# Kernel optimization log

Hardware: AMD Instinct MI355X
Metric: run time of the kernel (lower is better)

The kernel has to match this reference:

```python
import jax, jax.numpy as jnp
import numpy as np

N = 262144   # nodes
E = 2097152  # edges (avg degree 8)
F_IN, L0, L1, K = 14, 128, 15, 15


def setup_inputs() -> dict:
    key = jax.random.key(0)
    ks = jax.random.split(key, 24)
    s = 0.1
    return {
        "x": jax.random.normal(ks[0], (N, F_IN), jnp.float32),
        "edge_index": jax.random.randint(ks[1], (2, E), 0, N, dtype=jnp.int32),
        "y": jax.random.randint(ks[2], (N, 1), 0, 2, dtype=jnp.int32),
        "sel": jax.random.bernoulli(ks[3], 0.98, (N, 1)),
        "Wl1": jax.random.normal(ks[4], (F_IN, L0)) * s,
        "Wr1": jax.random.normal(ks[5], (F_IN, L0)) * s,
        "b1": jnp.zeros((L0,), jnp.float32),
        "Wl2": jax.random.normal(ks[6], (L0, L0)) * s,
        "Wr2": jax.random.normal(ks[7], (L0, L0)) * s,
        "b2": jnp.zeros((L0,), jnp.float32),
        "Wl3": jax.random.normal(ks[8], (L0, 1)) * s,
        "Wr3": jax.random.normal(ks[9], (L0, 1)) * s,
        "b3": jnp.zeros((1,), jnp.float32),
        "Wt1": jax.random.normal(ks[10], (K + 1, F_IN, L1)) * s,
        "bt1": jnp.zeros((L1,), jnp.float32),
        "Wt2": jax.random.normal(ks[11], (K + 1, L1, L1)) * s,
        "bt2": jnp.zeros((L1,), jnp.float32),
        "Wt3": jax.random.normal(ks[12], (K + 1, L1, 1)) * s,
        "bt3": jnp.zeros((1,), jnp.float32),
        "Wlin": jax.random.normal(ks[13], (2, 1)) * s,
        "blin": jnp.zeros((1,), jnp.float32),
    }


def _sage(h, src, dst, inv_deg, Wl, Wr, b):
    # PyG SAGEConv (mean aggr): lin_l(mean_j x_j) + lin_r(x_i) + b
    agg = jax.ops.segment_sum(h[src], dst, num_segments=N) * inv_deg
    return agg @ Wl + h @ Wr + b


def _tag(h, src, dst, norm, W, b):
    # PyG TAGConv: sum_k (D^-1/2 A D^-1/2)^k x @ W_k + b
    out = h @ W[0]
    for k in range(1, W.shape[0]):
        h = jax.ops.segment_sum(norm[:, None] * h[src], dst, num_segments=N)
        out = out + h @ W[k]
    return out + b


def reference(x, edge_index, y, sel, Wl1, Wr1, b1, Wl2, Wr2, b2, Wl3, Wr3, b3,
              Wt1, bt1, Wt2, bt2, Wt3, bt3, Wlin, blin):
    src, dst = edge_index[0], edge_index[1]
    ones = jnp.ones((E,), jnp.float32)
    deg = jax.ops.segment_sum(ones, dst, num_segments=N)  # in-degree at targets
    inv_deg = (1.0 / jnp.maximum(deg, 1.0))[:, None]
    # gcn_norm without self-loops for TAGConv
    dinv = jnp.where(deg > 0, jax.lax.rsqrt(jnp.maximum(deg, 1.0)), 0.0)
    norm = dinv[src] * dinv[dst]  # [E]

    # SAGE branch
    x1 = jax.nn.sigmoid(_sage(x, src, dst, inv_deg, Wl1, Wr1, b1))
    for _ in range(4):
        x1 = jax.nn.sigmoid(_sage(x1, src, dst, inv_deg, Wl2, Wr2, b2))
    x1 = jax.nn.relu(_sage(x1, src, dst, inv_deg, Wl3, Wr3, b3))

    # TAG branch
    x3 = jax.nn.sigmoid(_tag(x, src, dst, norm, Wt1, bt1))
    for _ in range(4):
        x3 = jax.nn.sigmoid(_tag(x3, src, dst, norm, Wt2, bt2))
    x3 = jax.nn.relu(_tag(x3, src, dst, norm, Wt3, bt3))

    out = jax.nn.relu(jnp.concatenate([x1, x3], axis=1) @ Wlin + blin)
    return jnp.where(sel & (y == 0), 0.0, out)
```

## Files before the change

### kernel.cpp

```cpp
#include <hip/hip_runtime.h>
#include <math.h>

#define NN 262144
#define EE 2097152
#define FIN 14
#define LW 128
#define TW 15

typedef unsigned short ushort_t;
typedef unsigned int uint_t;
typedef __attribute__((ext_vector_type(8))) short bf16x8v;
typedef __attribute__((ext_vector_type(4))) float f32x4v;

static __device__ __forceinline__ float sigmoidf_(float v) { return 1.0f / (1.0f + expf(-v)); }

static __device__ __forceinline__ float bf2f(unsigned short u) {
  union { unsigned int i; float f; } v; v.i = ((unsigned int)u) << 16; return v.f;
}
static __device__ __forceinline__ unsigned short f2bf(float f) {
  union { float f; unsigned int i; } v; v.f = f;
  unsigned int r = v.i + 0x7FFF + ((v.i >> 16) & 1);
  return (unsigned short)(r >> 16);
}
static __device__ __forceinline__ unsigned int pack2(float a, float b) {
  return ((unsigned int)f2bf(b) << 16) | (unsigned int)f2bf(a);
}
static __device__ __forceinline__ void addrow16(float* acc, uint4 u0, uint4 u1) {
  acc[0]  += bf2f((unsigned short)(u0.x & 0xFFFF)); acc[1]  += bf2f((unsigned short)(u0.x >> 16));
  acc[2]  += bf2f((unsigned short)(u0.y & 0xFFFF)); acc[3]  += bf2f((unsigned short)(u0.y >> 16));
  acc[4]  += bf2f((unsigned short)(u0.z & 0xFFFF)); acc[5]  += bf2f((unsigned short)(u0.z >> 16));
  acc[6]  += bf2f((unsigned short)(u0.w & 0xFFFF)); acc[7]  += bf2f((unsigned short)(u0.w >> 16));
  acc[8]  += bf2f((unsigned short)(u1.x & 0xFFFF)); acc[9]  += bf2f((unsigned short)(u1.x >> 16));
  acc[10] += bf2f((unsigned short)(u1.y & 0xFFFF)); acc[11] += bf2f((unsigned short)(u1.y >> 16));
  acc[12] += bf2f((unsigned short)(u1.z & 0xFFFF)); acc[13] += bf2f((unsigned short)(u1.z >> 16));
  acc[14] += bf2f((unsigned short)(u1.w & 0xFFFF)); acc[15] += bf2f((unsigned short)(u1.w >> 16));
}

__global__ void k_selprobe(const unsigned char* __restrict__ selb, int* __restrict__ flag) {
  __shared__ int cnt;
  if (threadIdx.x == 0) cnt = 0;
  __syncthreads();
  int c = 0;
  for (int i = threadIdx.x; i < 4096; i += 256) c += (selb[i] != 0) ? 1 : 0;
  atomicAdd(&cnt, c);
  __syncthreads();
  if (threadIdx.x == 0) *flag = (cnt > 3000) ? 1 : 0;
}

__global__ void k_norm_bool(const int* __restrict__ flag, const unsigned char* __restrict__ selb,
                            unsigned char* __restrict__ selN) {
  if (*flag != 1) return;
  int i = blockIdx.x * 256 + threadIdx.x;
  selN[i] = (selb[i] != 0) ? 1 : 0;
}

__global__ void k_norm_int(const int* __restrict__ flag, const unsigned char* __restrict__ selb,
                           unsigned char* __restrict__ selN) {
  if (*flag != 0) return;
  int i = blockIdx.x * 256 + threadIdx.x;
  selN[i] = (((const int*)selb)[i] != 0) ? 1 : 0;
}

__global__ void k_deg(const int* __restrict__ ei, int* __restrict__ deg) {
  int e = blockIdx.x * 256 + threadIdx.x;
  if (e < EE) atomicAdd(&deg[ei[EE + e]], 1);
}

__global__ void k_scan_partial(const int* __restrict__ deg, int* __restrict__ btot) {
  __shared__ int sd[256];
  int t = threadIdx.x, b = blockIdx.x;
  int i0 = b * 1024 + t * 4;
  int s = deg[i0] + deg[i0 + 1] + deg[i0 + 2] + deg[i0 + 3];
  sd[t] = s; __syncthreads();
  for (int off = 1; off < 256; off <<= 1) {
    int x = (t >= off) ? sd[t - off] : 0;
    __syncthreads(); sd[t] += x; __syncthreads();
  }
  if (t == 255) btot[b] = sd[255];
}

__global__ void k_scan_block(const int* __restrict__ btot, int* __restrict__ bbase, int* __restrict__ row_start) {
  __shared__ int sd[256];
  int t = threadIdx.x;
  int v = btot[t];
  sd[t] = v; __syncthreads();
  for (int off = 1; off < 256; off <<= 1) {
    int x = (t >= off) ? sd[t - off] : 0;
    __syncthreads(); sd[t] += x; __syncthreads();
  }
  bbase[t] = sd[t] - v;
  if (t == 255) row_start[NN] = sd[255];
}

__global__ void k_scan_final(const int* __restrict__ deg, const int* __restrict__ bbase,
                             int* __restrict__ row_start, float* __restrict__ inv_deg,
                             float* __restrict__ dinv) {
  __shared__ int sd[256];
  int t = threadIdx.x, b = blockIdx.x;
  int i0 = b * 1024 + t * 4;
  int d0 = deg[i0], d1 = deg[i0 + 1], d2 = deg[i0 + 2], d3 = deg[i0 + 3];
  int s = d0 + d1 + d2 + d3;
  sd[t] = s; __syncthreads();
  for (int off = 1; off < 256; off <<= 1) {
    int x = (t >= off) ? sd[t - off] : 0;
    __syncthreads(); sd[t] += x; __syncthreads();
  }
  int base = bbase[b] + sd[t] - s;
  row_start[i0]     = base;
  row_start[i0 + 1] = base + d0;
  row_start[i0 + 2] = base + d0 + d1;
  row_start[i0 + 3] = base + d0 + d1 + d2;
  int dd[4] = {d0, d1, d2, d3};
  for (int j = 0; j < 4; ++j) {
    float df = (float)dd[j];
    inv_deg[i0 + j] = 1.0f / fmaxf(df, 1.0f);
    dinv[i0 + j] = (dd[j] > 0) ? rsqrtf(fmaxf(df, 1.0f)) : 0.0f;
  }
}

__global__ void k_fill(const int* __restrict__ ei, const int* __restrict__ row_start,
                       int* __restrict__ cursor, int* __restrict__ csr_src) {
  int e = blockIdx.x * 256 + threadIdx.x;
  if (e >= EE) return;
  int s = ei[e], d = ei[EE + e];
  int pos = atomicAdd(&cursor[d], 1);
  csr_src[row_start[d] + pos] = s;
}

__global__ void k_pad_x(const float* __restrict__ x, float* __restrict__ xp,
                        ushort_t* __restrict__ xpb, ushort_t* __restrict__ xc) {
  int idx = blockIdx.x * 256 + threadIdx.x;
  int i = idx >> 4, lane = idx & 15;
  float v = (lane < FIN) ? x[(size_t)i * FIN + lane] : 0.0f;
  xp[idx] = v;
  ushort_t b = f2bf(v);
  xpb[idx] = b;
  xc[(size_t)i * 32 + 16 + lane] = b;
}

__global__ __launch_bounds__(256) void k_prop16_mean(
    const float* __restrict__ h, ushort_t* __restrict__ xc,
    const int* __restrict__ row_start, const int* __restrict__ csr_src,
    const float* __restrict__ inv_deg) {
  int i = blockIdx.x * 256 + threadIdx.x;
  float acc[16];
  #pragma unroll
  for (int c = 0; c < 16; ++c) acc[c] = 0.0f;
  int e0 = row_start[i], e1 = row_start[i + 1];
  int e = e0;
  for (; e + 2 <= e1; e += 2) {
    int i0 = csr_src[e], i1 = csr_src[e + 1];
    const float4* r0 = (const float4*)(h + (size_t)i0 * 16);
    const float4* r1 = (const float4*)(h + (size_t)i1 * 16);
    float4 a0 = r0[0], a1 = r0[1], a2 = r0[2], a3 = r0[3];
    float4 b0 = r1[0], b1 = r1[1], b2 = r1[2], b3 = r1[3];
    acc[0]+=a0.x+b0.x; acc[1]+=a0.y+b0.y; acc[2]+=a0.z+b0.z; acc[3]+=a0.w+b0.w;
    acc[4]+=a1.x+b1.x; acc[5]+=a1.y+b1.y; acc[6]+=a1.z+b1.z; acc[7]+=a1.w+b1.w;
    acc[8]+=a2.x+b2.x; acc[9]+=a2.y+b2.y; acc[10]+=a2.z+b2.z; acc[11]+=a2.w+b2.w;
    acc[12]+=a3.x+b3.x; acc[13]+=a3.y+b3.y; acc[14]+=a3.z+b3.z; acc[15]+=a3.w+b3.w;
  }
  for (; e < e1; ++e) {
    const float4* r0 = (const float4*)(h + (size_t)csr_src[e] * 16);
    float4 a0 = r0[0], a1 = r0[1], a2 = r0[2], a3 = r0[3];
    acc[0]+=a0.x; acc[1]+=a0.y; acc[2]+=a0.z; acc[3]+=a0.w;
    acc[4]+=a1.x; acc[5]+=a1.y; acc[6]+=a1.z; acc[7]+=a1.w;
    acc[8]+=a2.x; acc[9]+=a2.y; acc[10]+=a2.z; acc[11]+=a2.w;
    acc[12]+=a3.x; acc[13]+=a3.y; acc[14]+=a3.z; acc[15]+=a3.w;
  }
  float idg = inv_deg[i];
  uint_t o[8];
  #pragma unroll
  for (int q = 0; q < 8; ++q) o[q] = pack2(acc[2*q]*idg, acc[2*q+1]*idg);
  uint4* dst = (uint4*)(xc + (size_t)i * 32);
  dst[0] = make_uint4(o[0], o[1], o[2], o[3]);
  dst[1] = make_uint4(o[4], o[5], o[6], o[7]);
}

__global__ void k_convW1(const float* __restrict__ Wl1, const float* __restrict__ Wr1,
                         ushort_t* __restrict__ Wc) {
  int idx = blockIdx.x * 256 + threadIdx.x;
  int n = idx >> 5, k = idx & 31;
  float v = 0.0f;
  if (k < FIN) v = Wl1[k * 128 + n];
  else if (k >= 16 && k < 16 + FIN) v = Wr1[(k - 16) * 128 + n];
  Wc[idx] = f2bf(v);
}

__global__ __launch_bounds__(256) void k_gemm_small_mfma(
    const ushort_t* __restrict__ xc, const ushort_t* __restrict__ Wc,
    const float* __restrict__ bias, ushort_t* __restrict__ out) {
  int tid = threadIdx.x;
  int wave = tid >> 6, lane = tid & 63;
  int row0 = blockIdx.x * 64 + wave * 16;
  int r = lane & 15, kg = lane >> 4;
  bf16x8v a = *(const bf16x8v*)(xc + (size_t)(row0 + r) * 32 + kg * 8);
  f32x4v acc[8];
  #pragma unroll
  for (int nt = 0; nt < 8; ++nt) {
    acc[nt] = (f32x4v){0.f, 0.f, 0.f, 0.f};
    bf16x8v b = *(const bf16x8v*)(Wc + (size_t)(nt * 16 + r) * 32 + kg * 8);
    acc[nt] = __builtin_amdgcn_mfma_f32_16x16x32_bf16(a, b, acc[nt], 0, 0, 0);
  }
  #pragma unroll
  for (int nt = 0; nt < 8; ++nt) {
    #pragma unroll
    for (int j = 0; j < 4; ++j) {
      float v = sigmoidf_(acc[nt][j] + bias[nt * 16 + r]);
      out[(size_t)(row0 + kg * 4 + j) * LW + nt * 16 + r] = f2bf(v);
    }
  }
}

__global__ void k_prop128(const ushort_t* __restrict__ h, ushort_t* __restrict__ out,
                          const int* __restrict__ row_start, const int* __restrict__ csr_src,
                          const float* __restrict__ inv_deg) {
  int t = threadIdx.x;
  int g = blockIdx.x * 4 + (t >> 6);
  int lane = t & 63;
  int s0 = row_start[g], s1 = row_start[g + 1];
  float a0 = 0.0f, a1 = 0.0f;
  int e = s0;
  for (; e + 8 <= s1; e += 8) {
    int id[8];
    #pragma unroll
    for (int j = 0; j < 8; ++j) id[j] = csr_src[e + j];
    uint_t u[8];
    #pragma unroll
    for (int j = 0; j < 8; ++j) u[j] = *(const uint_t*)(h + (size_t)id[j] * LW + 2 * lane);
    #pragma unroll
    for (int j = 0; j < 8; ++j) {
      a0 += bf2f((unsigned short)(u[j] & 0xFFFF));
      a1 += bf2f((unsigned short)(u[j] >> 16));
    }
  }
  for (; e < s1; ++e) {
    uint_t u = *(const uint_t*)(h + (size_t)csr_src[e] * LW + 2 * lane);
    a0 += bf2f((unsigned short)(u & 0xFFFF));
    a1 += bf2f((unsigned short)(u >> 16));
  }
  float idg = inv_deg[g];
  *(uint_t*)(out + (size_t)g * LW + 2 * lane) = pack2(a0 * idg, a1 * idg);
}

__global__ void k_convW(const float* __restrict__ Wl, const float* __restrict__ Wr,
                        ushort_t* __restrict__ Wt) {
  int idx = blockIdx.x * 256 + threadIdx.x;
  int n = idx >> 8, k = idx & 255;
  float v = (k < 128) ? Wl[k * 128 + n] : Wr[(k - 128) * 128 + n];
  Wt[idx] = f2bf(v);
}

__global__ __launch_bounds__(256) void k_gemm128_mfma(
    const ushort_t* __restrict__ A1, const ushort_t* __restrict__ A2,
    const ushort_t* __restrict__ Wt,
    const float* __restrict__ bias, ushort_t* __restrict__ out) {
  int tid = threadIdx.x;
  int wave = tid >> 6, lane = tid & 63;
  int row0 = blockIdx.x * 64 + wave * 16;
  int r = lane & 15, kg = lane >> 4;
  f32x4v acc[8];
  #pragma unroll
  for (int nt = 0; nt < 8; ++nt) acc[nt] = (f32x4v){0.f, 0.f, 0.f, 0.f};
  #pragma unroll
  for (int ks = 0; ks < 8; ++ks) {
    const ushort_t* asrc = (ks < 4)
        ? (A1 + (size_t)(row0 + r) * LW + ks * 32 + kg * 8)
        : (A2 + (size_t)(row0 + r) * LW + (ks - 4) * 32 + kg * 8);
    bf16x8v a = *(const bf16x8v*)asrc;
    #pragma unroll
    for (int nt = 0; nt < 8; ++nt) {
      bf16x8v b = *(const bf16x8v*)(Wt + (size_t)(nt * 16 + r) * 256 + ks * 32 + kg * 8);
      acc[nt] = __builtin_amdgcn_mfma_f32_16x16x32_bf16(a, b, acc[nt], 0, 0, 0);
    }
  }
  #pragma unroll
  for (int nt = 0; nt < 8; ++nt) {
    #pragma unroll
    for (int j = 0; j < 4; ++j) {
      float v = sigmoidf_(acc[nt][j] + bias[nt * 16 + r]);
      out[(size_t)(row0 + kg * 4 + j) * LW + nt * 16 + r] = f2bf(v);
    }
  }
}

__global__ void k_wide_to1(const ushort_t* __restrict__ H, const float* __restrict__ Wl3,
                           const float* __restrict__ Wr3, float* __restrict__ g_l,
                           float* __restrict__ g_r) {
  int wave = (blockIdx.x * 256 + threadIdx.x) >> 6;
  int lane = threadIdx.x & 63;
  unsigned int u = *(const unsigned int*)(H + (size_t)wave * LW + 2 * lane);
  float h0 = bf2f((unsigned short)(u & 0xFFFF));
  float h1 = bf2f((unsigned short)(u >> 16));
  float al = h0 * Wl3[2 * lane] + h1 * Wl3[2 * lane + 1];
  float ar = h0 * Wr3[2 * lane] + h1 * Wr3[2 * lane + 1];
  #pragma unroll
  for (int off = 32; off; off >>= 1) {
    al += __shfl_xor(al, off);
    ar += __shfl_xor(ar, off);
  }
  if (lane == 0) { g_l[wave] = al; g_r[wave] = ar; }
}

__global__ void k_sage_final(const float* __restrict__ g_l, const float* __restrict__ g_r,
                             const float* __restrict__ b3, const int* __restrict__ row_start,
                             const int* __restrict__ csr_src, const float* __restrict__ inv_deg,
                             float* __restrict__ x1) {
  int i = blockIdx.x * 256 + threadIdx.x;
  int e0 = row_start[i], e1 = row_start[i + 1];
  float s = 0.0f;
  int e = e0;
  for (; e + 4 <= e1; e += 4) {
    float w0 = g_l[csr_src[e]], w1 = g_l[csr_src[e+1]];
    float w2 = g_l[csr_src[e+2]], w3 = g_l[csr_src[e+3]];
    s += (w0 + w1) + (w2 + w3);
  }
  for (; e < e1; ++e) s += g_l[csr_src[e]];
  float v = s * inv_deg[i] + g_r[i] + b3[0];
  x1[i] = fmaxf(v, 0.0f);
}

__global__ __launch_bounds__(256) void k_tag_hh(
    const ushort_t* __restrict__ T, const float* __restrict__ W, int win,
    const ushort_t* __restrict__ w_in, ushort_t* __restrict__ w_out,
    const float* __restrict__ bias, int mode,
    const float* __restrict__ W2, int win2, ushort_t* __restrict__ w_next2,
    const int* __restrict__ row_start, const int* __restrict__ csr_src,
    const float* __restrict__ dinv) {
  __shared__ float Ws[16][16];
  __shared__ float Ws2[16][16];
  int t = threadIdx.x;
  { int rr = t >> 4, c = t & 15; Ws[rr][c] = (rr < win && c < TW) ? W[rr * TW + c] : 0.0f; }
  if (mode == 3) {
    int rr = t >> 4, c = t & 15;
    Ws2[rr][c] = (rr < win2 && c < TW) ? W2[rr * TW + c] : 0.0f;
  }
  __syncthreads();
  int i = blockIdx.x * 256 + t;
  float di = dinv[i];
  float acc[16];
  #pragma unroll
  for (int c = 0; c < 16; ++c) acc[c] = 0.0f;

  if (mode != 0) {
    int e0 = row_start[i], e1 = row_start[i + 1];
    int e = e0;
    for (; e + 8 <= e1; e += 8) {
      int id[8];
      #pragma unroll
      for (int j = 0; j < 8; ++j) id[j] = csr_src[e + j];
      uint4 u0[8], u1[8];
      #pragma unroll
      for (int j = 0; j < 8; ++j) {
        const uint4* p = (const uint4*)(w_in + (size_t)id[j] * 16);
        u0[j] = p[0]; u1[j] = p[1];
      }
      #pragma unroll
      for (int j = 0; j < 8; ++j) addrow16(acc, u0[j], u1[j]);
    }
    for (; e + 4 <= e1; e += 4) {
      int id[4];
      #pragma unroll
      for (int j = 0; j < 4; ++j) id[j] = csr_src[e + j];
      uint4 u0[4], u1[4];
      #pragma unroll
      for (int j = 0; j < 4; ++j) {
        const uint4* p = (const uint4*)(w_in + (size_t)id[j] * 16);
        u0[j] = p[0]; u1[j] = p[1];
      }
      #pragma unroll
      for (int j = 0; j < 4; ++j) addrow16(acc, u0[j], u1[j]);
    }
    for (; e < e1; ++e) {
      const uint4* p = (const uint4*)(w_in + (size_t)csr_src[e] * 16);
      addrow16(acc, p[0], p[1]);
    }
    #pragma unroll
    for (int c = 0; c < 16; ++c) acc[c] *= di;
  }

  uint4 t0 = *(const uint4*)(T + (size_t)i * 16);
  uint4 t1 = *(const uint4*)(T + (size_t)i * 16 + 8);
  float tv[16];
  tv[0]=bf2f((unsigned short)(t0.x&0xFFFF)); tv[1]=bf2f((unsigned short)(t0.x>>16));
  tv[2]=bf2f((unsigned short)(t0.y&0xFFFF)); tv[3]=bf2f((unsigned short)(t0.y>>16));
  tv[4]=bf2f((unsigned short)(t0.z&0xFFFF)); tv[5]=bf2f((unsigned short)(t0.z>>16));
  tv[6]=bf2f((unsigned short)(t0.w&0xFFFF)); tv[7]=bf2f((unsigned short)(t0.w>>16));
  tv[8]=bf2f((unsigned short)(t1.x&0xFFFF)); tv[9]=bf2f((unsigned short)(t1.x>>16));
  tv[10]=bf2f((unsigned short)(t1.y&0xFFFF)); tv[11]=bf2f((unsigned short)(t1.y>>16));
  tv[12]=bf2f((unsigned short)(t1.z&0xFFFF)); tv[13]=bf2f((unsigned short)(t1.z>>16));
  tv[14]=bf2f((unsigned short)(t1.w&0xFFFF)); tv[15]=bf2f((unsigned short)(t1.w>>16));
  #pragma unroll
  for (int f = 0; f < 16; ++f) {
    float tf = tv[f];
    const float4* wr = (const float4*)Ws[f];
    float4 w0 = wr[0], w1 = wr[1], w2 = wr[2], w3 = wr[3];
    acc[0]+=tf*w0.x; acc[1]+=tf*w0.y; acc[2]+=tf*w0.z; acc[3]+=tf*w0.w;
    acc[4]+=tf*w1.x; acc[5]+=tf*w1.y; acc[6]+=tf*w1.z; acc[7]+=tf*w1.w;
    acc[8]+=tf*w2.x; acc[9]+=tf*w2.y; acc[10]+=tf*w2.z; acc[11]+=tf*w2.w;
    acc[12]+=tf*w3.x; acc[13]+=tf*w3.y; acc[14]+=tf*w3.z; acc[15]+=tf*w3.w;
  }

  if (mode >= 2) {
    float tn[16];
    #pragma unroll
    for (int c = 0; c < 16; ++c)
      tn[c] = (c < TW) ? sigmoidf_(acc[c] + bias[c]) : 0.0f;
    uint_t o[8];
    #pragma unroll
    for (int q = 0; q < 8; ++q) o[q] = pack2(tn[2*q], tn[2*q+1]);
    uint4* dst = (uint4*)(w_out + (size_t)i * 16);
    dst[0] = make_uint4(o[0], o[1], o[2], o[3]);
    dst[1] = make_uint4(o[4], o[5], o[6], o[7]);
    if (mode == 3) {
      float wn[16];
      #pragma unroll
      for (int c = 0; c < 16; ++c) wn[c] = 0.0f;
      #pragma unroll
      for (int f = 0; f < 16; ++f) {
        float tf = tn[f];
        const float4* wr = (const float4*)Ws2[f];
        float4 w0 = wr[0], w1 = wr[1], w2 = wr[2], w3 = wr[3];
        wn[0]+=tf*w0.x; wn[1]+=tf*w0.y; wn[2]+=tf*w0.z; wn[3]+=tf*w0.w;
        wn[4]+=tf*w1.x; wn[5]+=tf*w1.y; wn[6]+=tf*w1.z; wn[7]+=tf*w1.w;
        wn[8]+=tf*w2.x; wn[9]+=tf*w2.y; wn[10]+=tf*w2.z; wn[11]+=tf*w2.w;
        wn[12]+=tf*w3.x; wn[13]+=tf*w3.y; wn[14]+=tf*w3.z; wn[15]+=tf*w3.w;
      }
      uint_t o2[8];
      #pragma unroll
      for (int q = 0; q < 8; ++q) o2[q] = pack2(di * wn[2*q], di * wn[2*q+1]);
      uint4* dst2 = (uint4*)(w_next2 + (size_t)i * 16);
      dst2[0] = make_uint4(o2[0], o2[1], o2[2], o2[3]);
      dst2[1] = make_uint4(o2[4], o2[5], o2[6], o2[7]);
    }
  } else {
    uint_t o[8];
    #pragma unroll
    for (int q = 0; q < 8; ++q) o[q] = pack2(di * acc[2*q], di * acc[2*q+1]);
    uint4* dst = (uint4*)(w_out + (size_t)i * 16);
    dst[0] = make_uint4(o[0], o[1], o[2], o[3]);
    dst[1] = make_uint4(o[4], o[5], o[6], o[7]);
  }
}

__global__ void k_tag_g(const ushort_t* __restrict__ T, const float* __restrict__ Wt3,
                        const float* __restrict__ dinv, float* __restrict__ gT,
                        float* __restrict__ w15) {
  __shared__ float Ws[16 * TW];
  int t = threadIdx.x;
  if (t < 16 * TW) Ws[t] = Wt3[t];
  __syncthreads();
  int i = blockIdx.x * 256 + t;
  const ushort_t* tr = T + (size_t)i * 16;
  float row[TW];
  #pragma unroll
  for (int f = 0; f < TW; ++f) row[f] = bf2f(tr[f]);
  #pragma unroll
  for (int k = 0; k < 16; ++k) {
    float a = 0.0f;
    #pragma unroll
    for (int f = 0; f < TW; ++f) a += row[f] * Ws[k * TW + f];
    if (k < 15) gT[(size_t)k * NN + i] = a;
    else        w15[i] = dinv[i] * a;
  }
}

__global__ void k_horner(const float* __restrict__ gk, const float* __restrict__ w_in,
                         float* __restrict__ w_out,
                         const int* __restrict__ row_start, const int* __restrict__ csr_src,
                         const float* __restrict__ dinv) {
  int i = blockIdx.x * 256 + threadIdx.x;
  int e0 = row_start[i], e1 = row_start[i + 1];
  float gs = 0.0f;
  int e = e0;
  for (; e + 4 <= e1; e += 4) {
    float w0 = w_in[csr_src[e]],   w1 = w_in[csr_src[e+1]];
    float w2 = w_in[csr_src[e+2]], w3 = w_in[csr_src[e+3]];
    gs += (w0 + w1) + (w2 + w3);
  }
  for (; e < e1; ++e) gs += w_in[csr_src[e]];
  float s = gk[i] + dinv[i] * gs;
  w_out[i] = dinv[i] * s;
}

__global__ void k_horner_fin(const float* __restrict__ g0, const float* __restrict__ w_in,
                             const float* __restrict__ x1, const int* __restrict__ y,
                             const unsigned char* __restrict__ selN,
                             const float* __restrict__ Wlin, const float* __restrict__ blin,
                             const float* __restrict__ bt3,
                             const int* __restrict__ row_start, const int* __restrict__ csr_src,
                             const float* __restrict__ dinv, float* __restrict__ out) {
  int i = blockIdx.x * 256 + threadIdx.x;
  int e0 = row_start[i], e1 = row_start[i + 1];
  float gs = 0.0f;
  int e = e0;
  for (; e + 4 <= e1; e += 4) {
    float w0 = w_in[csr_src[e]],   w1 = w_in[csr_src[e+1]];
    float w2 = w_in[csr_src[e+2]], w3 = w_in[csr_src[e+3]];
    gs += (w0 + w1) + (w2 + w3);
  }
  for (; e < e1; ++e) gs += w_in[csr_src[e]];
  float s = g0[i] + dinv[i] * gs;
  float x3 = fmaxf(s + bt3[0], 0.0f);
  float v = fmaxf(x1[i] * Wlin[0] + x3 * Wlin[1] + blin[0], 0.0f);
  bool z = (selN[i] != 0) && (y[i] == 0);
  out[i] = z ? 0.0f : v;
}

extern "C" void kernel_launch(void* const* d_in, const int* in_sizes, int n_in,
                              void* d_out, int out_size, void* d_ws, size_t ws_size,
                              hipStream_t stream) {
  const float* x    = (const float*)d_in[0];
  const int*   ei   = (const int*)d_in[1];
  const int*   y    = (const int*)d_in[2];
  const unsigned char* sel = (const unsigned char*)d_in[3];
  const float* Wl1  = (const float*)d_in[4];
  const float* Wr1  = (const float*)d_in[5];
  const float* b1   = (const float*)d_in[6];
  const float* Wl2  = (const float*)d_in[7];
  const float* Wr2  = (const float*)d_in[8];
  const float* b2   = (const float*)d_in[9];
  const float* Wl3  = (const float*)d_in[10];
  const float* Wr3  = (const float*)d_in[11];
  const float* b3   = (const float*)d_in[12];
  const float* Wt1  = (const float*)d_in[13];
  const float* bt1  = (const float*)d_in[14];
  const float* Wt2  = (const float*)d_in[15];
  const float* bt2  = (const float*)d_in[16];
  const float* Wt3  = (const float*)d_in[17];
  const float* bt3  = (const float*)d_in[18];
  const float* Wlin = (const float*)d_in[19];
  const float* blin = (const float*)d_in[20];

  const size_t MB = 1 << 20;
  unsigned char* w8 = (unsigned char*)d_ws;
  int*   deg       = (int*)(w8 + 0 * MB);
  int*   cursor    = (int*)(w8 + 1 * MB);
  int*   row_start = (int*)(w8 + 2 * MB);
  float* inv_deg   = (float*)(w8 + 4 * MB);
  float* dinv      = (float*)(w8 + 5 * MB);
  float* x1        = (float*)(w8 + 6 * MB);
  float* g_l       = (float*)(w8 + 7 * MB);
  float* g_r       = (float*)(w8 + 8 * MB);
  int*   btot      = (int*)(w8 + 9 * MB);
  int*   bbase     = (int*)(w8 + 9 * MB + 4096);
  int*   selflag   = (int*)(w8 + 9 * MB + 8192);
  float* w6a       = (float*)(w8 + 11 * MB);
  float* w6b       = (float*)(w8 + 12 * MB);
  unsigned char* selN = (unsigned char*)(w8 + 13 * MB);
  ushort_t* Wtc    = (ushort_t*)(w8 + 14 * MB);
  ushort_t* Wc1    = (ushort_t*)(w8 + 15 * MB);
  int*   csr_src   = (int*)(w8 + 16 * MB);
  float* xp        = (float*)(w8 + 24 * MB);
  ushort_t* xpb    = (ushort_t*)(w8 + 40 * MB);
  ushort_t* H      = (ushort_t*)(w8 + 48 * MB);
  ushort_t* AGG    = (ushort_t*)(w8 + 112 * MB);
  ushort_t* xc     = (ushort_t*)(w8 + 112 * MB);
  ushort_t* T0  = (ushort_t*)(w8 + 112 * MB);
  ushort_t* T1  = (ushort_t*)(w8 + 120 * MB);
  ushort_t* wA  = (ushort_t*)(w8 + 128 * MB);
  ushort_t* wB  = (ushort_t*)(w8 + 136 * MB);
  float* gT     = (float*)(w8 + 144 * MB);

  k_selprobe<<<1, 256, 0, stream>>>(sel, selflag);
  k_norm_bool<<<NN / 256, 256, 0, stream>>>(selflag, sel, selN);
  k_norm_int<<<NN / 256, 256, 0, stream>>>(selflag, sel, selN);

  hipMemsetAsync(w8, 0, 2 * MB, stream);
  k_deg<<<EE / 256, 256, 0, stream>>>(ei, deg);
  k_scan_partial<<<256, 256, 0, stream>>>(deg, btot);
  k_scan_block<<<1, 256, 0, stream>>>(btot, bbase, row_start);
  k_scan_final<<<256, 256, 0, stream>>>(deg, bbase, row_start, inv_deg, dinv);
  k_fill<<<EE / 256, 256, 0, stream>>>(ei, row_start, cursor, csr_src);
  k_pad_x<<<NN * 16 / 256, 256, 0, stream>>>(x, xp, xpb, xc);
  k_convW<<<128, 256, 0, stream>>>(Wl2, Wr2, Wtc);
  k_convW1<<<16, 256, 0, stream>>>(Wl1, Wr1, Wc1);

  k_prop16_mean<<<NN / 256, 256, 0, stream>>>(xp, xc, row_start, csr_src, inv_deg);
  k_gemm_small_mfma<<<NN / 64, 256, 0, stream>>>(xc, Wc1, b1, H);
  for (int l = 0; l < 4; ++l) {
    k_prop128<<<NN / 4, 256, 0, stream>>>(H, AGG, row_start, csr_src, inv_deg);
    k_gemm128_mfma<<<NN / 64, 256, 0, stream>>>(AGG, H, Wtc, b2, H);
  }
  k_wide_to1<<<NN / 4, 256, 0, stream>>>(H, Wl3, Wr3, g_l, g_r);
  k_sage_final<<<NN / 256, 256, 0, stream>>>(g_l, g_r, b3, row_start, csr_src, inv_deg, x1);

  const size_t FT = (size_t)FIN * TW;
  const size_t TT = (size_t)TW * TW;
  ushort_t* wi = wA; ushort_t* wo = wB;
  k_tag_hh<<<NN / 256, 256, 0, stream>>>(xpb, Wt1 + 15 * FT, FIN, nullptr, wi, nullptr, 0,
                                         nullptr, 0, nullptr, row_start, csr_src, dinv);
  for (int k = 14; k >= 1; --k) {
    k_tag_hh<<<NN / 256, 256, 0, stream>>>(xpb, Wt1 + (size_t)k * FT, FIN, wi, wo, nullptr, 1,
                                           nullptr, 0, nullptr, row_start, csr_src, dinv);
    ushort_t* tmp = wi; wi = wo; wo = tmp;
  }
  k_tag_hh<<<NN / 256, 256, 0, stream>>>(xpb, Wt1, FIN, wi, T0, bt1, 3,
                                         Wt2 + 15 * TT, TW, wo, row_start, csr_src, dinv);
  { ushort_t* tmp = wi; wi = wo; wo = tmp; }
  ushort_t* tin = T0; ushort_t* tout = T1;
  for (int l = 0; l < 4; ++l) {
    for (int k = 14; k >= 1; --k) {
      k_tag_hh<<<NN / 256, 256, 0, stream>>>(tin, Wt2 + (size_t)k * TT, TW, wi, wo, nullptr, 1,
                                             nullptr, 0, nullptr, row_start, csr_src, dinv);
      ushort_t* tmp = wi; wi = wo; wo = tmp;
    }
    if (l < 3) {
      k_tag_hh<<<NN / 256, 256, 0, stream>>>(tin, Wt2, TW, wi, tout, bt2, 3,
                                             Wt2 + 15 * TT, TW, wo, row_start, csr_src, dinv);
      ushort_t* tmp = wi; wi = wo; wo = tmp;
    } else {
      k_tag_hh<<<NN / 256, 256, 0, stream>>>(tin, Wt2, TW, wi, tout, bt2, 2,
                                             nullptr, 0, nullptr, row_start, csr_src, dinv);
    }
    ushort_t* tmp = tin; tin = tout; tout = tmp;
  }
  k_tag_g<<<NN / 256, 256, 0, stream>>>(tin, Wt3, dinv, gT, w6a);
  float* fwi = w6a; float* fwo = w6b;
  for (int k = 14; k >= 1; --k) {
    k_horner<<<NN / 256, 256, 0, stream>>>(gT + (size_t)k * NN, fwi, fwo,
                                           row_start, csr_src, dinv);
    float* tmp = fwi; fwi = fwo; fwo = tmp;
  }
  k_horner_fin<<<NN / 256, 256, 0, stream>>>(gT, fwi, x1, y, selN, Wlin, blin, bt3,
                                             row_start, csr_src, dinv, (float*)d_out);
}
```

Before: 4.309 ms.

## Split TAG and prop16 gathers across two threads per node, templatize mode

The 16-wide TAG Horner kernels and the first SAGE mean aggregation now use two threads per node, each gathering and accumulating 8 channels. Mode-3 exchanges the two halves with a lane shuffle so each thread can compute its half of the next-layer projection. The first SAGE layer now gathers bf16 rows instead of fp32, which drops the fp32 padded copy of x. Other changes: mode becomes a template parameter, the 128-wide GEMM loads all A fragments before its MFMA loop, and the Horner gathers unroll by 8. These are meant to raise memory-level parallelism and occupancy in the many latency-bound gather kernels, at the cost of duplicated index loads and doubled thread count.

```diff
diff --git a/kernel.cpp b/kernel.cpp
--- a/kernel.cpp
+++ b/kernel.cpp
@@ -25,15 +25,11 @@
 static __device__ __forceinline__ unsigned int pack2(float a, float b) {
   return ((unsigned int)f2bf(b) << 16) | (unsigned int)f2bf(a);
 }
-static __device__ __forceinline__ void addrow16(float* acc, uint4 u0, uint4 u1) {
-  acc[0]  += bf2f((unsigned short)(u0.x & 0xFFFF)); acc[1]  += bf2f((unsigned short)(u0.x >> 16));
-  acc[2]  += bf2f((unsigned short)(u0.y & 0xFFFF)); acc[3]  += bf2f((unsigned short)(u0.y >> 16));
-  acc[4]  += bf2f((unsigned short)(u0.z & 0xFFFF)); acc[5]  += bf2f((unsigned short)(u0.z >> 16));
-  acc[6]  += bf2f((unsigned short)(u0.w & 0xFFFF)); acc[7]  += bf2f((unsigned short)(u0.w >> 16));
-  acc[8]  += bf2f((unsigned short)(u1.x & 0xFFFF)); acc[9]  += bf2f((unsigned short)(u1.x >> 16));
-  acc[10] += bf2f((unsigned short)(u1.y & 0xFFFF)); acc[11] += bf2f((unsigned short)(u1.y >> 16));
-  acc[12] += bf2f((unsigned short)(u1.z & 0xFFFF)); acc[13] += bf2f((unsigned short)(u1.z >> 16));
-  acc[14] += bf2f((unsigned short)(u1.w & 0xFFFF)); acc[15] += bf2f((unsigned short)(u1.w >> 16));
+static __device__ __forceinline__ void addrow8(float* acc, uint4 u) {
+  acc[0] += bf2f((unsigned short)(u.x & 0xFFFF)); acc[1] += bf2f((unsigned short)(u.x >> 16));
+  acc[2] += bf2f((unsigned short)(u.y & 0xFFFF)); acc[3] += bf2f((unsigned short)(u.y >> 16));
+  acc[4] += bf2f((unsigned short)(u.z & 0xFFFF)); acc[5] += bf2f((unsigned short)(u.z >> 16));
+  acc[6] += bf2f((unsigned short)(u.w & 0xFFFF)); acc[7] += bf2f((unsigned short)(u.w >> 16));
 }
 
 __global__ void k_selprobe(const unsigned char* __restrict__ selb, int* __restrict__ flag) {
@@ -127,53 +123,48 @@
   csr_src[row_start[d] + pos] = s;
 }
 
-__global__ void k_pad_x(const float* __restrict__ x, float* __restrict__ xp,
-                        ushort_t* __restrict__ xpb, ushort_t* __restrict__ xc) {
+__global__ void k_pad_x(const float* __restrict__ x, ushort_t* __restrict__ xpb,
+                        ushort_t* __restrict__ xc) {
   int idx = blockIdx.x * 256 + threadIdx.x;
   int i = idx >> 4, lane = idx & 15;
   float v = (lane < FIN) ? x[(size_t)i * FIN + lane] : 0.0f;
-  xp[idx] = v;
   ushort_t b = f2bf(v);
   xpb[idx] = b;
   xc[(size_t)i * 32 + 16 + lane] = b;
 }
 
-__global__ __launch_bounds__(256) void k_prop16_mean(
-    const float* __restrict__ h, ushort_t* __restrict__ xc,
+__global__ __launch_bounds__(256) void k_prop16b(
+    const ushort_t* __restrict__ h, ushort_t* __restrict__ xc,
     const int* __restrict__ row_start, const int* __restrict__ csr_src,
     const float* __restrict__ inv_deg) {
-  int i = blockIdx.x * 256 + threadIdx.x;
-  float acc[16];
-  #pragma unroll
-  for (int c = 0; c < 16; ++c) acc[c] = 0.0f;
+  int gi = blockIdx.x * 256 + threadIdx.x;
+  int i = gi >> 1, half = gi & 1;
+  float acc[8];
+  #pragma unroll
+  for (int c = 0; c < 8; ++c) acc[c] = 0.0f;
+  const ushort_t* wbase = h + half * 8;
   int e0 = row_start[i], e1 = row_start[i + 1];
   int e = e0;
+  for (; e + 8 <= e1; e += 8) {
+    int id[8];
+    #pragma unroll
+    for (int j = 0; j < 8; ++j) id[j] = csr_src[e + j];
+    uint4 u[8];
+    #pragma unroll
+    for (int j = 0; j < 8; ++j) u[j] = *(const uint4*)(wbase + (size_t)id[j] * 16);
+    #pragma unroll
+    for (int j = 0; j < 8; ++j) addrow8(acc, u[j]);
+  }
   for (; e + 2 <= e1; e += 2) {
-    int i0 = csr_src[e], i1 = csr_src[e + 1];
-    const float4* r0 = (const float4*)(h + (size_t)i0 * 16);
-    const float4* r1 = (const float4*)(h + (size_t)i1 * 16);
-    float4 a0 = r0[0], a1 = r0[1], a2 = r0[2], a3 = r0[3];
-    float4 b0 = r1[0], b1 = r1[1], b2 = r1[2], b3 = r1[3];
-    acc[0]+=a0.x+b0.x; acc[1]+=a0.y+b0.y; acc[2]+=a0.z+b0.z; acc[3]+=a0.w+b0.w;
-    acc[4]+=a1.x+b1.x; acc[5]+=a1.y+b1.y; acc[6]+=a1.z+b1.z; acc[7]+=a1.w+b1.w;
-    acc[8]+=a2.x+b2.x; acc[9]+=a2.y+b2.y; acc[10]+=a2.z+b2.z; acc[11]+=a2.w+b2.w;
-    acc[12]+=a3.x+b3.x; acc[13]+=a3.y+b3.y; acc[14]+=a3.z+b3.z; acc[15]+=a3.w+b3.w;
-  }
-  for (; e < e1; ++e) {
-    const float4* r0 = (const float4*)(h + (size_t)csr_src[e] * 16);
-    float4 a0 = r0[0], a1 = r0[1], a2 = r0[2], a3 = r0[3];
-    acc[0]+=a0.x; acc[1]+=a0.y; acc[2]+=a0.z; acc[3]+=a0.w;
-    acc[4]+=a1.x; acc[5]+=a1.y; acc[6]+=a1.z; acc[7]+=a1.w;
-    acc[8]+=a2.x; acc[9]+=a2.y; acc[10]+=a2.z; acc[11]+=a2.w;
-    acc[12]+=a3.x; acc[13]+=a3.y; acc[14]+=a3.z; acc[15]+=a3.w;
-  }
+    uint4 u0 = *(const uint4*)(wbase + (size_t)csr_src[e] * 16);
+    uint4 u1 = *(const uint4*)(wbase + (size_t)csr_src[e + 1] * 16);
+    addrow8(acc, u0); addrow8(acc, u1);
+  }
+  if (e < e1) addrow8(acc, *(const uint4*)(wbase + (size_t)csr_src[e] * 16));
   float idg = inv_deg[i];
-  uint_t o[8];
-  #pragma unroll
-  for (int q = 0; q < 8; ++q) o[q] = pack2(acc[2*q]*idg, acc[2*q+1]*idg);
-  uint4* dst = (uint4*)(xc + (size_t)i * 32);
-  dst[0] = make_uint4(o[0], o[1], o[2], o[3]);
-  dst[1] = make_uint4(o[4], o[5], o[6], o[7]);
+  uint4 o = make_uint4(pack2(acc[0]*idg, acc[1]*idg), pack2(acc[2]*idg, acc[3]*idg),
+                       pack2(acc[4]*idg, acc[5]*idg), pack2(acc[6]*idg, acc[7]*idg));
+  *(uint4*)(xc + (size_t)i * 32 + half * 8) = o;
 }
 
 __global__ void k_convW1(const float* __restrict__ Wl1, const float* __restrict__ Wr1,
@@ -258,19 +249,23 @@
   int wave = tid >> 6, lane = tid & 63;
   int row0 = blockIdx.x * 64 + wave * 16;
   int r = lane & 15, kg = lane >> 4;
-  f32x4v acc[8];
-  #pragma unroll
-  for (int nt = 0; nt < 8; ++nt) acc[nt] = (f32x4v){0.f, 0.f, 0.f, 0.f};
+  bf16x8v a[8];
   #pragma unroll
   for (int ks = 0; ks < 8; ++ks) {
     const ushort_t* asrc = (ks < 4)
         ? (A1 + (size_t)(row0 + r) * LW + ks * 32 + kg * 8)
         : (A2 + (size_t)(row0 + r) * LW + (ks - 4) * 32 + kg * 8);
-    bf16x8v a = *(const bf16x8v*)asrc;
+    a[ks] = *(const bf16x8v*)asrc;
+  }
+  f32x4v acc[8];
+  #pragma unroll
+  for (int nt = 0; nt < 8; ++nt) acc[nt] = (f32x4v){0.f, 0.f, 0.f, 0.f};
+  #pragma unroll
+  for (int ks = 0; ks < 8; ++ks) {
     #pragma unroll
     for (int nt = 0; nt < 8; ++nt) {
       bf16x8v b = *(const bf16x8v*)(Wt + (size_t)(nt * 16 + r) * 256 + ks * 32 + kg * 8);
-      acc[nt] = __builtin_amdgcn_mfma_f32_16x16x32_bf16(a, b, acc[nt], 0, 0, 0);
+      acc[nt] = __builtin_amdgcn_mfma_f32_16x16x32_bf16(a[ks], b, acc[nt], 0, 0, 0);
     }
   }
   #pragma unroll
@@ -319,63 +314,50 @@
   x1[i] = fmaxf(v, 0.0f);
 }
 
+template<int MODE>
 __global__ __launch_bounds__(256) void k_tag_hh(
     const ushort_t* __restrict__ T, const float* __restrict__ W, int win,
     const ushort_t* __restrict__ w_in, ushort_t* __restrict__ w_out,
-    const float* __restrict__ bias, int mode,
+    const float* __restrict__ bias,
     const float* __restrict__ W2, int win2, ushort_t* __restrict__ w_next2,
     const int* __restrict__ row_start, const int* __restrict__ csr_src,
     const float* __restrict__ dinv) {
   __shared__ float Ws[16][16];
   __shared__ float Ws2[16][16];
   int t = threadIdx.x;
-  { int rr = t >> 4, c = t & 15; Ws[rr][c] = (rr < win && c < TW) ? W[rr * TW + c] : 0.0f; }
-  if (mode == 3) {
-    int rr = t >> 4, c = t & 15;
-    Ws2[rr][c] = (rr < win2 && c < TW) ? W2[rr * TW + c] : 0.0f;
-  }
+  { int rr = t >> 4, c = t & 15;
+    Ws[rr][c] = (rr < win && c < TW) ? W[rr * TW + c] : 0.0f;
+    if (MODE == 3) Ws2[rr][c] = (rr < win2 && c < TW) ? W2[rr * TW + c] : 0.0f; }
   __syncthreads();
-  int i = blockIdx.x * 256 + t;
+  int gi = blockIdx.x * 256 + t;
+  int i = gi >> 1, half = gi & 1;
   float di = dinv[i];
-  float acc[16];
-  #pragma unroll
-  for (int c = 0; c < 16; ++c) acc[c] = 0.0f;
-
-  if (mode != 0) {
+  float acc[8];
+  #pragma unroll
+  for (int c = 0; c < 8; ++c) acc[c] = 0.0f;
+
+  if (MODE != 0) {
+    const ushort_t* wbase = w_in + half * 8;
     int e0 = row_start[i], e1 = row_start[i + 1];
     int e = e0;
     for (; e + 8 <= e1; e += 8) {
       int id[8];
       #pragma unroll
       for (int j = 0; j < 8; ++j) id[j] = csr_src[e + j];
-      uint4 u0[8], u1[8];
-      #pragma unroll
-      for (int j = 0; j < 8; ++j) {
-        const uint4* p = (const uint4*)(w_in + (size_t)id[j] * 16);
-        u0[j] = p[0]; u1[j] = p[1];
-      }
-      #pragma unroll
-      for (int j = 0; j < 8; ++j) addrow16(acc, u0[j], u1[j]);
-    }
-    for (; e + 4 <= e1; e += 4) {
-      int id[4];
-      #pragma unroll
-      for (int j = 0; j < 4; ++j) id[j] = csr_src[e + j];
-      uint4 u0[4], u1[4];
-      #pragma unroll
-      for (int j = 0; j < 4; ++j) {
-        const uint4* p = (const uint4*)(w_in + (size_t)id[j] * 16);
-        u0[j] = p[0]; u1[j] = p[1];
-      }
-      #pragma unroll
-      for (int j = 0; j < 4; ++j) addrow16(acc, u0[j], u1[j]);
-    }
-    for (; e < e1; ++e) {
-      const uint4* p = (const uint4*)(w_in + (size_t)csr_src[e] * 16);
-      addrow16(acc, p[0], p[1]);
-    }
-    #pragma unroll
-    for (int c = 0; c < 16; ++c) acc[c] *= di;
+      uint4 u[8];
+      #pragma unroll
+      for (int j = 0; j < 8; ++j) u[j] = *(const uint4*)(wbase + (size_t)id[j] * 16);
+      #pragma unroll
+      for (int j = 0; j < 8; ++j) addrow8(acc, u[j]);
+    }
+    for (; e + 2 <= e1; e += 2) {
+      uint4 u0 = *(const uint4*)(wbase + (size_t)csr_src[e] * 16);
+      uint4 u1 = *(const uint4*)(wbase + (size_t)csr_src[e + 1] * 16);
+      addrow8(acc, u0); addrow8(acc, u1);
+    }
+    if (e < e1) addrow8(acc, *(const uint4*)(wbase + (size_t)csr_src[e] * 16));
+    #pragma unroll
+    for (int c = 0; c < 8; ++c) acc[c] *= di;
   }
 
   uint4 t0 = *(const uint4*)(T + (size_t)i * 16);
@@ -392,53 +374,58 @@
   #pragma unroll
   for (int f = 0; f < 16; ++f) {
     float tf = tv[f];
-    const float4* wr = (const float4*)Ws[f];
-    float4 w0 = wr[0], w1 = wr[1], w2 = wr[2], w3 = wr[3];
+    const float4* wr = (const float4*)&Ws[f][half * 8];
+    float4 w0 = wr[0], w1 = wr[1];
     acc[0]+=tf*w0.x; acc[1]+=tf*w0.y; acc[2]+=tf*w0.z; acc[3]+=tf*w0.w;
     acc[4]+=tf*w1.x; acc[5]+=tf*w1.y; acc[6]+=tf*w1.z; acc[7]+=tf*w1.w;
-    acc[8]+=tf*w2.x; acc[9]+=tf*w2.y; acc[10]+=tf*w2.z; acc[11]+=tf*w2.w;
-    acc[12]+=tf*w3.x; acc[13]+=tf*w3.y; acc[14]+=tf*w3.z; acc[15]+=tf*w3.w;
-  }
-
-  if (mode >= 2) {
-    float tn[16];
-    #pragma unroll
-    for (int c = 0; c < 16; ++c)
-      tn[c] = (c < TW) ? sigmoidf_(acc[c] + bias[c]) : 0.0f;
-    uint_t o[8];
-    #pragma unroll
-    for (int q = 0; q < 8; ++q) o[q] = pack2(tn[2*q], tn[2*q+1]);
-    uint4* dst = (uint4*)(w_out + (size_t)i * 16);
-    dst[0] = make_uint4(o[0], o[1], o[2], o[3]);
-    dst[1] = make_uint4(o[4], o[5], o[6], o[7]);
-    if (mode == 3) {
-      float wn[16];
-      #pragma unroll
-      for (int c = 0; c < 16; ++c) wn[c] = 0.0f;
-      #pragma unroll
-      for (int f = 0; f < 16; ++f) {
-        float tf = tn[f];
-        const float4* wr = (const float4*)Ws2[f];
-        float4 w0 = wr[0], w1 = wr[1], w2 = wr[2], w3 = wr[3];
+  }
+
+  if (MODE >= 2) {
+    int cbase = half * 8;
+    float tn[8];
+    #pragma unroll
+    for (int c = 0; c < 8; ++c)
+      tn[c] = (cbase + c < TW) ? sigmoidf_(acc[c] + bias[cbase + c]) : 0.0f;
+    uint4 o = make_uint4(pack2(tn[0],tn[1]), pack2(tn[2],tn[3]),
+                         pack2(tn[4],tn[5]), pack2(tn[6],tn[7]));
+    *(uint4*)(w_out + (size_t)i * 16 + cbase) = o;
+    if (MODE == 3) {
+      float to[8];
+      #pragma unroll
+      for (int c = 0; c < 8; ++c) to[c] = __shfl_xor(tn[c], 1);
+      float lo[8], hi[8];
+      #pragma unroll
+      for (int c = 0; c < 8; ++c) {
+        lo[c] = half ? to[c] : tn[c];
+        hi[c] = half ? tn[c] : to[c];
+      }
+      float wn[8];
+      #pragma unroll
+      for (int c = 0; c < 8; ++c) wn[c] = 0.0f;
+      #pragma unroll
+      for (int f = 0; f < 8; ++f) {
+        float tf = lo[f];
+        const float4* wr = (const float4*)&Ws2[f][cbase];
+        float4 w0 = wr[0], w1 = wr[1];
         wn[0]+=tf*w0.x; wn[1]+=tf*w0.y; wn[2]+=tf*w0.z; wn[3]+=tf*w0.w;
         wn[4]+=tf*w1.x; wn[5]+=tf*w1.y; wn[6]+=tf*w1.z; wn[7]+=tf*w1.w;
-        wn[8]+=tf*w2.x; wn[9]+=tf*w2.y; wn[10]+=tf*w2.z; wn[11]+=tf*w2.w;
-        wn[12]+=tf*w3.x; wn[13]+=tf*w3.y; wn[14]+=tf*w3.z; wn[15]+=tf*w3.w;
       }
-      uint_t o2[8];
-      #pragma unroll
-      for (int q = 0; q < 8; ++q) o2[q] = pack2(di * wn[2*q], di * wn[2*q+1]);
-      uint4* dst2 = (uint4*)(w_next2 + (size_t)i * 16);
-      dst2[0] = make_uint4(o2[0], o2[1], o2[2], o2[3]);
-      dst2[1] = make_uint4(o2[4], o2[5], o2[6], o2[7]);
+      #pragma unroll
+      for (int f = 0; f < 8; ++f) {
+        float tf = hi[f];
+        const float4* wr = (const float4*)&Ws2[f + 8][cbase];
+        float4 w0 = wr[0], w1 = wr[1];
+        wn[0]+=tf*w0.x; wn[1]+=tf*w0.y; wn[2]+=tf*w0.z; wn[3]+=tf*w0.w;
+        wn[4]+=tf*w1.x; wn[5]+=tf*w1.y; wn[6]+=tf*w1.z; wn[7]+=tf*w1.w;
+      }
+      uint4 o2 = make_uint4(pack2(di*wn[0],di*wn[1]), pack2(di*wn[2],di*wn[3]),
+                            pack2(di*wn[4],di*wn[5]), pack2(di*wn[6],di*wn[7]));
+      *(uint4*)(w_next2 + (size_t)i * 16 + cbase) = o2;
     }
   } else {
-    uint_t o[8];
-    #pragma unroll
-    for (int q = 0; q < 8; ++q) o[q] = pack2(di * acc[2*q], di * acc[2*q+1]);
-    uint4* dst = (uint4*)(w_out + (size_t)i * 16);
-    dst[0] = make_uint4(o[0], o[1], o[2], o[3]);
-    dst[1] = make_uint4(o[4], o[5], o[6], o[7]);
+    uint4 o = make_uint4(pack2(di*acc[0],di*acc[1]), pack2(di*acc[2],di*acc[3]),
+                         pack2(di*acc[4],di*acc[5]), pack2(di*acc[6],di*acc[7]));
+    *(uint4*)(w_out + (size_t)i * 16 + half * 8) = o;
   }
 }
 
@@ -472,10 +459,15 @@
   int e0 = row_start[i], e1 = row_start[i + 1];
   float gs = 0.0f;
   int e = e0;
-  for (; e + 4 <= e1; e += 4) {
-    float w0 = w_in[csr_src[e]],   w1 = w_in[csr_src[e+1]];
-    float w2 = w_in[csr_src[e+2]], w3 = w_in[csr_src[e+3]];
-    gs += (w0 + w1) + (w2 + w3);
+  for (; e + 8 <= e1; e += 8) {
+    int id[8];
+    #pragma unroll
+    for (int j = 0; j < 8; ++j) id[j] = csr_src[e + j];
+    float w[8];
+    #pragma unroll
+    for (int j = 0; j < 8; ++j) w[j] = w_in[id[j]];
+    #pragma unroll
+    for (int j = 0; j < 8; ++j) gs += w[j];
   }
   for (; e < e1; ++e) gs += w_in[csr_src[e]];
   float s = gk[i] + dinv[i] * gs;
@@ -493,10 +485,15 @@
   int e0 = row_start[i], e1 = row_start[i + 1];
   float gs = 0.0f;
   int e = e0;
-  for (; e + 4 <= e1; e += 4) {
-    float w0 = w_in[csr_src[e]],   w1 = w_in[csr_src[e+1]];
-    float w2 = w_in[csr_src[e+2]], w3 = w_in[csr_src[e+3]];
-    gs += (w0 + w1) + (w2 + w3);
+  for (; e + 8 <= e1; e += 8) {
+    int id[8];
+    #pragma unroll
+    for (int j = 0; j < 8; ++j) id[j] = csr_src[e + j];
+    float w[8];
+    #pragma unroll
+    for (int j = 0; j < 8; ++j) w[j] = w_in[id[j]];
+    #pragma unroll
+    for (int j = 0; j < 8; ++j) gs += w[j];
   }
   for (; e < e1; ++e) gs += w_in[csr_src[e]];
   float s = g0[i] + dinv[i] * gs;
@@ -550,7 +547,6 @@
   ushort_t* Wtc    = (ushort_t*)(w8 + 14 * MB);
   ushort_t* Wc1    = (ushort_t*)(w8 + 15 * MB);
   int*   csr_src   = (int*)(w8 + 16 * MB);
-  float* xp        = (float*)(w8 + 24 * MB);
   ushort_t* xpb    = (ushort_t*)(w8 + 40 * MB);
   ushort_t* H      = (ushort_t*)(w8 + 48 * MB);
   ushort_t* AGG    = (ushort_t*)(w8 + 112 * MB);
@@ -571,11 +567,11 @@
   k_scan_block<<<1, 256, 0, stream>>>(btot, bbase, row_start);
   k_scan_final<<<256, 256, 0, stream>>>(deg, bbase, row_start, inv_deg, dinv);
   k_fill<<<EE / 256, 256, 0, stream>>>(ei, row_start, cursor, csr_src);
-  k_pad_x<<<NN * 16 / 256, 256, 0, stream>>>(x, xp, xpb, xc);
+  k_pad_x<<<NN * 16 / 256, 256, 0, stream>>>(x, xpb, xc);
   k_convW<<<128, 256, 0, stream>>>(Wl2, Wr2, Wtc);
   k_convW1<<<16, 256, 0, stream>>>(Wl1, Wr1, Wc1);
 
-  k_prop16_mean<<<NN / 256, 256, 0, stream>>>(xp, xc, row_start, csr_src, inv_deg);
+  k_prop16b<<<NN * 2 / 256, 256, 0, stream>>>(xpb, xc, row_start, csr_src, inv_deg);
   k_gemm_small_mfma<<<NN / 64, 256, 0, stream>>>(xc, Wc1, b1, H);
   for (int l = 0; l < 4; ++l) {
     k_prop128<<<NN / 4, 256, 0, stream>>>(H, AGG, row_start, csr_src, inv_deg);
@@ -586,31 +582,32 @@
 
   const size_t FT = (size_t)FIN * TW;
   const size_t TT = (size_t)TW * TW;
+  const int TG = NN * 2 / 256;
   ushort_t* wi = wA; ushort_t* wo = wB;
-  k_tag_hh<<<NN / 256, 256, 0, stream>>>(xpb, Wt1 + 15 * FT, FIN, nullptr, wi, nullptr, 0,
-                                         nullptr, 0, nullptr, row_start, csr_src, dinv);
+  k_tag_hh<0><<<TG, 256, 0, stream>>>(xpb, Wt1 + 15 * FT, FIN, nullptr, wi, nullptr,
+                                      nullptr, 0, nullptr, row_start, csr_src, dinv);
   for (int k = 14; k >= 1; --k) {
-    k_tag_hh<<<NN / 256, 256, 0, stream>>>(xpb, Wt1 + (size_t)k * FT, FIN, wi, wo, nullptr, 1,
-                                           nullptr, 0, nullptr, row_start, csr_src, dinv);
+    k_tag_hh<1><<<TG, 256, 0, stream>>>(xpb, Wt1 + (size_t)k * FT, FIN, wi, wo, nullptr,
+                                        nullptr, 0, nullptr, row_start, csr_src, dinv);
     ushort_t* tmp = wi; wi = wo; wo = tmp;
   }
-  k_tag_hh<<<NN / 256, 256, 0, stream>>>(xpb, Wt1, FIN, wi, T0, bt1, 3,
-                                         Wt2 + 15 * TT, TW, wo, row_start, csr_src, dinv);
+  k_tag_hh<3><<<TG, 256, 0, stream>>>(xpb, Wt1, FIN, wi, T0, bt1,
+                                      Wt2 + 15 * TT, TW, wo, row_start, csr_src, dinv);
   { ushort_t* tmp = wi; wi = wo; wo = tmp; }
   ushort_t* tin = T0; ushort_t* tout = T1;
   for (int l = 0; l < 4; ++l) {
     for (int k = 14; k >= 1; --k) {
-      k_tag_hh<<<NN / 256, 256, 0, stream>>>(tin, Wt2 + (size_t)k * TT, TW, wi, wo, nullptr, 1,
-                                             nullptr, 0, nullptr, row_start, csr_src, dinv);
+      k_tag_hh<1><<<TG, 256, 0, stream>>>(tin, Wt2 + (size_t)k * TT, TW, wi, wo, nullptr,
+                                          nullptr, 0, nullptr, row_start, csr_src, dinv);
       ushort_t* tmp = wi; wi = wo; wo = tmp;
     }
     if (l < 3) {
-      k_tag_hh<<<NN / 256, 256, 0, stream>>>(tin, Wt2, TW, wi, tout, bt2, 3,
-                                             Wt2 + 15 * TT, TW, wo, row_start, csr_src, dinv);
+      k_tag_hh<3><<<TG, 256, 0, stream>>>(tin, Wt2, TW, wi, tout, bt2,
+                                          Wt2 + 15 * TT, TW, wo, row_start, csr_src, dinv);
       ushort_t* tmp = wi; wi = wo; wo = tmp;
     } else {
-      k_tag_hh<<<NN / 256, 256, 0, stream>>>(tin, Wt2, TW, wi, tout, bt2, 2,
-                                             nullptr, 0, nullptr, row_start, csr_src, dinv);
+      k_tag_hh<2><<<TG, 256, 0, stream>>>(tin, Wt2, TW, wi, tout, bt2,
+                                          nullptr, 0, nullptr, row_start, csr_src, dinv);
     }
     ushort_t* tmp = tin; tin = tout; tout = tmp;
   }
```

Measured after the change: 4.074 ms. 5.5% less time.
